# Kernel tuning notes

Hardware: AMD Instinct MI355X
Metric: run time of the kernel (lower is better)

The kernel has to match this reference:

```python
import jax, jax.numpy as jnp
import numpy as np

EMB = 64
N_CONS = 100000
N_VARS = 200000
N_EDGES = 2000000


def _embed(x, shift, scale, W1, b1, W2, b2):
    # PreNormLayer (affine) -> Linear -> ReLU -> Linear -> ReLU
    x = (x - shift) * scale
    x = jax.nn.relu(x @ W1 + b1)
    return jax.nn.relu(x @ W2 + b2)


def _biconv(left, right, ei0, ei1, edge_lin, tgt_idx, n_tgt, tgt_feats,
            Wl, bl, Wr, sf, Wf, bf, sp, Woa, boa, Wob, bob):
    # gather-transform: per-edge joint features [E, EMB]
    joint = (left @ Wl + bl)[ei0] + edge_lin + (right @ Wr)[ei1]
    # feature_module_final: PreNorm(scale-only) -> ReLU -> Linear
    msg = jax.nn.relu(joint * sf) @ Wf + bf
    # scatter-add to target nodes, then post-conv PreNorm(scale-only)
    agg = jax.ops.segment_sum(msg, tgt_idx, num_segments=n_tgt) * sp
    h = jax.nn.relu(jnp.concatenate([agg, tgt_feats], axis=1) @ Woa + boa)
    return h @ Wob + bob


def _forward(constraint_features, edge_features, variable_features,
             c_shift, c_scale, c_W1, c_b1, c_W2, c_b2,
             v_shift, v_scale, v_W1, v_b1, v_W2, v_b2,
             e_shift, e_scale,
             vc_Wl, vc_bl, vc_We, vc_Wr, vc_sf, vc_Wf, vc_bf, vc_sp,
             vc_Woa, vc_boa, vc_Wob, vc_bob,
             cv_Wl, cv_bl, cv_We, cv_Wr, cv_sf, cv_Wf, cv_bf, cv_sp,
             cv_Woa, cv_boa, cv_Wob, cv_bob,
             out_W1, out_b1, out_W2, edge_indices):
    ei0, ei1 = edge_indices[0], edge_indices[1]
    c = _embed(constraint_features, c_shift, c_scale, c_W1, c_b1, c_W2, c_b2)
    v = _embed(variable_features, v_shift, v_scale, v_W1, v_b1, v_W2, v_b2)
    e = (edge_features - e_shift) * e_scale  # edge embedding = PreNorm only, dim 1
    # conv_v_to_c (right_to_left=True): target = constraints via ei0
    c = jax.nn.relu(_biconv(c, v, ei0, ei1, e @ vc_We, ei0, N_CONS, c,
                            vc_Wl, vc_bl, vc_Wr, vc_sf, vc_Wf, vc_bf, vc_sp,
                            vc_Woa, vc_boa, vc_Wob, vc_bob))
    # conv_c_to_v: target = variables via ei1
    v = jax.nn.relu(_biconv(c, v, ei0, ei1, e @ cv_We, ei1, N_VARS, v,
                            cv_Wl, cv_bl, cv_Wr, cv_sf, cv_Wf, cv_bf, cv_sp,
                            cv_Woa, cv_boa, cv_Wob, cv_bob))
    out = jax.nn.relu(v @ out_W1 + out_b1) @ out_W2  # [N_VARS, 1]
    return out.reshape(1, -1)


def setup_inputs():
    key = jax.random.key(0)
    ks = iter(jax.random.split(key, 64))

    def rn(shape, s=0.1):
        return (jax.random.normal(next(ks), shape, jnp.float32) * s).astype(jnp.float32)

    d = {}
    d["constraint_features"] = rn((N_CONS, 5), 1.0)
    d["edge_features"] = rn((N_EDGES, 1), 1.0)
    d["variable_features"] = rn((N_VARS, 19), 1.0)

    def prenorm(n, pre):
        d[pre + "shift"] = rn((n,), 0.05)
        d[pre + "scale"] = jnp.ones((n,), jnp.float32) + rn((n,), 0.05)

    prenorm(5, "c_"); prenorm(19, "v_"); prenorm(1, "e_")
    for pre, nin in (("c_", 5), ("v_", 19)):
        d[pre + "W1"] = rn((nin, EMB)); d[pre + "b1"] = rn((EMB,), 0.02)
        d[pre + "W2"] = rn((EMB, EMB)); d[pre + "b2"] = rn((EMB,), 0.02)
    for pre in ("vc_", "cv_"):
        d[pre + "Wl"] = rn((EMB, EMB)); d[pre + "bl"] = rn((EMB,), 0.02)
        d[pre + "We"] = rn((1, EMB)); d[pre + "Wr"] = rn((EMB, EMB))
        d[pre + "sf"] = jnp.float32(1.0) + rn((), 0.05)
        d[pre + "Wf"] = rn((EMB, EMB)); d[pre + "bf"] = rn((EMB,), 0.02)
        d[pre + "sp"] = jnp.float32(1.0) + rn((), 0.05)
        d[pre + "Woa"] = rn((2 * EMB, EMB)); d[pre + "boa"] = rn((EMB,), 0.02)
        d[pre + "Wob"] = rn((EMB, EMB)); d[pre + "bob"] = rn((EMB,), 0.02)
    d["out_W1"] = rn((EMB, EMB)); d["out_b1"] = rn((EMB,), 0.02)
    d["out_W2"] = rn((EMB, 1))
    d["edge_indices"] = jnp.stack([
        jax.random.randint(next(ks), (N_EDGES,), 0, N_CONS),
        jax.random.randint(next(ks), (N_EDGES,), 0, N_VARS)]).astype(jnp.int32)
    d["n_cons_per_sample"] = jnp.array([N_CONS], jnp.int32)
    d["n_vars_per_sample"] = jnp.array([N_VARS], jnp.int32)
    return d


def reference(constraint_features, edge_features, variable_features,
              c_shift, c_scale, c_W1, c_b1, c_W2, c_b2,
              v_shift, v_scale, v_W1, v_b1, v_W2, v_b2,
              e_shift, e_scale,
              vc_Wl, vc_bl, vc_We, vc_Wr, vc_sf, vc_Wf, vc_bf, vc_sp,
              vc_Woa, vc_boa, vc_Wob, vc_bob,
              cv_Wl, cv_bl, cv_We, cv_Wr, cv_sf, cv_Wf, cv_bf, cv_sp,
              cv_Woa, cv_boa, cv_Wob, cv_bob,
              out_W1, out_b1, out_W2,
              edge_indices, n_cons_per_sample, n_vars_per_sample):
    return _forward(constraint_features, edge_features, variable_features,
                    c_shift, c_scale, c_W1, c_b1, c_W2, c_b2,
                    v_shift, v_scale, v_W1, v_b1, v_W2, v_b2,
                    e_shift, e_scale,
                    vc_Wl, vc_bl, vc_We, vc_Wr, vc_sf, vc_Wf, vc_bf, vc_sp,
                    vc_Woa, vc_boa, vc_Wob, vc_bob,
                    cv_Wl, cv_bl, cv_We, cv_Wr, cv_sf, cv_Wf, cv_bf, cv_sp,
                    cv_Woa, cv_boa, cv_Wob, cv_bob,
                    out_W1, out_b1, out_W2, edge_indices)
```

## Files before the change

kernel.cpp:

```cpp
#include <hip/hip_runtime.h>
#include <hip/hip_bf16.h>

#define DEV __device__ __forceinline__

typedef __attribute__((ext_vector_type(8))) short short8;
typedef __attribute__((ext_vector_type(4))) float f32x4;

DEV unsigned short f2bf(float f) {
    __hip_bfloat16 h = __float2bfloat16(f);
    unsigned short u;
    __builtin_memcpy(&u, &h, 2);
    return u;
}
DEV float bf2f(unsigned short u) { return __uint_as_float((unsigned int)u << 16); }

DEV f32x4 mfma_bf16(short8 a, short8 b, f32x4 c) {
    return __builtin_amdgcn_mfma_f32_16x16x32_bf16(a, b, c, 0, 0, 0);
}

DEV void make_hilo(const float* a8, short8& hi, short8& lo) {
    #pragma unroll
    for (int j = 0; j < 8; ++j) {
        const float v = a8[j];
        const unsigned short h = f2bf(v);
        hi[j] = (short)h;
        lo[j] = (short)f2bf(v - bf2f(h));
    }
}

DEV void mfma3(f32x4 acc[4], short8 ah, short8 al,
               const unsigned short* __restrict__ Bh,
               const unsigned short* __restrict__ Bl,
               int nkt, int tidx, int lane) {
    #pragma unroll
    for (int c = 0; c < 4; ++c) {
        const size_t o = ((size_t)(c * nkt + tidx) * 64 + lane) * 8;
        const short8 bh = *(const short8*)(Bh + o);
        const short8 bl = *(const short8*)(Bl + o);
        acc[c] = mfma_bf16(ah, bh, acc[c]);
        acc[c] = mfma_bf16(al, bh, acc[c]);
        acc[c] = mfma_bf16(ah, bl, acc[c]);
    }
}

DEV int swf(int row, int col) {
    return row * 64 + ((((col >> 3) ^ row) & 7) << 3) + (col & 7);
}

DEV void gemm_lds(f32x4 acc[4], const float* Xl,
                  const unsigned short* Bh, const unsigned short* Bl,
                  int nkt, int t0, int ntk, int l15, int q, int lane) {
    for (int t = 0; t < ntk; ++t) {
        const int ch = (t * 4 + q) ^ (l15 & 7);
        const float* a8 = Xl + l15 * 64 + ch * 8;
        short8 ah, al;
        make_hilo(a8, ah, al);
        mfma3(acc, ah, al, Bh, Bl, nkt, t0 + t, lane);
    }
}

DEV void gemm_glb(f32x4 acc[4], const float* __restrict__ Xg, int rbase, int N,
                  const unsigned short* Bh, const unsigned short* Bl,
                  int nkt, int t0, int ntk, int l15, int q, int lane) {
    const int grow = rbase + l15;
    const bool ok = grow < N;
    for (int t = 0; t < ntk; ++t) {
        float a8[8];
        if (ok) {
            const float4 v0 = *(const float4*)(Xg + (size_t)grow * 64 + t * 32 + q * 8);
            const float4 v1 = *(const float4*)(Xg + (size_t)grow * 64 + t * 32 + q * 8 + 4);
            a8[0] = v0.x; a8[1] = v0.y; a8[2] = v0.z; a8[3] = v0.w;
            a8[4] = v1.x; a8[5] = v1.y; a8[6] = v1.z; a8[7] = v1.w;
        } else {
            #pragma unroll
            for (int j = 0; j < 8; ++j) a8[j] = 0.f;
        }
        short8 ah, al;
        make_hilo(a8, ah, al);
        mfma3(acc, ah, al, Bh, Bl, nkt, t0 + t, lane);
    }
}

#define NMAT 15
struct PrepArgs {
    const float* src[NMAT];
    unsigned short* hi[NMAT];
    unsigned short* lo[NMAT];
    int nkt[NMAT];
    int KR[NMAT];
};

__global__ __launch_bounds__(256)
void prep_kernel(PrepArgs pa)
{
    const int m = blockIdx.y;
    const int nkt = pa.nkt[m];
    const int nthr = nkt * 4 * 64;
    const int p = blockIdx.x * 256 + threadIdx.x;
    if (p >= nthr) return;
    const int f = p >> 6, l = p & 63;
    const int c = f / nkt, t = f % nkt;
    const int kbase = t * 32 + ((l >> 4) << 3);
    const int n = c * 16 + (l & 15);
    const float* W = pa.src[m];
    const int KR = pa.KR[m];
    unsigned short* ph = pa.hi[m] + (size_t)p * 8;
    unsigned short* pl = pa.lo[m] + (size_t)p * 8;
    #pragma unroll
    for (int j = 0; j < 8; ++j) {
        const int k = kbase + j;
        const float v = (k < KR) ? W[k * 64 + n] : 0.f;
        const unsigned short h = f2bf(v);
        ph[j] = h;
        pl[j] = f2bf(v - bf2f(h));
    }
}

struct FusedArgs {
    const int* ei; int E; int nH;
    int* h1; int* h2; unsigned int* rank;
    int tC, tV;
    const float* cf; int NC;
    const float* c_shift; const float* c_scale;
    const float* vf; int NV;
    const float* v_shift; const float* v_scale;
    const unsigned short *cW1h, *cW1l, *cW2h, *cW2l, *cWt1h, *cWt1l;
    const unsigned short *vW1h, *vW1l, *vW2h, *vW2l, *vWt1h, *vWt1l, *vWt2h, *vWt2l;
    const float *c_b1, *c_b2, *v_b1, *v_b2, *vc_bl;
    const float *vc_sf, *cv_sf;
    float* Emc; float* Emv;
    unsigned short* A1; unsigned short* B1; unsigned short* B2;
};

__global__ __launch_bounds__(256)
void fused_he_kernel(FusedArgs a)
{
    __shared__ __align__(16) float Bb[4][1024];

    const int half = blockIdx.x & 1;
    const int idx  = blockIdx.x >> 1;

    if (half == 0) {
        const int stride = a.nH * 256;
        for (int e = idx * 256 + (int)threadIdx.x; e < a.E; e += stride) {
            const int r1 = atomicAdd(a.h1 + a.ei[e], 1);
            const int r2 = atomicAdd(a.h2 + a.ei[a.E + e], 1);
            a.rank[e] = (unsigned int)r1 | ((unsigned int)r2 << 16);
        }
        return;
    }

    int tile = idx;
    const float* x; int N; int IN;
    const float *shift, *scale, *b1, *b2, *bt1;
    const unsigned short *W1h, *W1l, *W2h, *W2l, *Wt1h, *Wt1l;
    const unsigned short *Wt2h = nullptr, *Wt2l = nullptr;
    float* Em; unsigned short* T1; unsigned short* T2 = nullptr;
    float sf1, sf2 = 0.f;
    if (tile < a.tC) {
        x = a.cf; N = a.NC; IN = 5; shift = a.c_shift; scale = a.c_scale;
        W1h = a.cW1h; W1l = a.cW1l; b1 = a.c_b1;
        W2h = a.cW2h; W2l = a.cW2l; b2 = a.c_b2;
        Em = a.Emc; Wt1h = a.cWt1h; Wt1l = a.cWt1l; bt1 = a.vc_bl;
        sf1 = a.vc_sf[0]; T1 = a.A1;
    } else {
        tile -= a.tC;
        x = a.vf; N = a.NV; IN = 19; shift = a.v_shift; scale = a.v_scale;
        W1h = a.vW1h; W1l = a.vW1l; b1 = a.v_b1;
        W2h = a.vW2h; W2l = a.vW2l; b2 = a.v_b2;
        Em = a.Emv; Wt1h = a.vWt1h; Wt1l = a.vWt1l; bt1 = nullptr;
        sf1 = a.vc_sf[0]; T1 = a.B1;
        Wt2h = a.vWt2h; Wt2l = a.vWt2l; sf2 = a.cv_sf[0]; T2 = a.B2;
    }

    const int w = threadIdx.x >> 6, lane = threadIdx.x & 63;
    const int l15 = lane & 15, q = lane >> 4;
    const int rbase = tile * 64 + w * 16;

    {
        f32x4 acc[4] = {{0,0,0,0},{0,0,0,0},{0,0,0,0},{0,0,0,0}};
        const int grow = rbase + l15;
        float a8[8];
        #pragma unroll
        for (int j = 0; j < 8; ++j) {
            const int col = q * 8 + j;
            float v = 0.f;
            if (grow < N && col < IN) v = (x[(size_t)grow * IN + col] - shift[col]) * scale[col];
            a8[j] = v;
        }
        short8 ah, al;
        make_hilo(a8, ah, al);
        mfma3(acc, ah, al, W1h, W1l, 1, 0, lane);
        #pragma unroll
        for (int c = 0; c < 4; ++c) {
            const int col = c * 16 + l15;
            const float bb = b1[col];
            #pragma unroll
            for (int r = 0; r < 4; ++r)
                Bb[w][swf(q * 4 + r, col)] = fmaxf(acc[c][r] + bb, 0.f);
        }
    }
    {
        f32x4 acc[4] = {{0,0,0,0},{0,0,0,0},{0,0,0,0},{0,0,0,0}};
        gemm_lds(acc, Bb[w], W2h, W2l, 2, 0, 2, l15, q, lane);
        #pragma unroll
        for (int c = 0; c < 4; ++c) {
            const int col = c * 16 + l15;
            const float bb = b2[col];
            #pragma unroll
            for (int r = 0; r < 4; ++r) {
                const int row = q * 4 + r;
                const int grow = rbase + row;
                const float v = fmaxf(acc[c][r] + bb, 0.f);
                Bb[w][swf(row, col)] = v;
                if (grow < N) Em[(size_t)grow * 64 + col] = v;
            }
        }
    }
    {
        f32x4 acc[4] = {{0,0,0,0},{0,0,0,0},{0,0,0,0},{0,0,0,0}};
        gemm_lds(acc, Bb[w], Wt1h, Wt1l, 2, 0, 2, l15, q, lane);
        #pragma unroll
        for (int c = 0; c < 4; ++c) {
            const int col = c * 16 + l15;
            const float bb = bt1 ? bt1[col] : 0.f;
            #pragma unroll
            for (int r = 0; r < 4; ++r) {
                const int grow = rbase + q * 4 + r;
                if (grow < N) T1[(size_t)grow * 64 + col] = f2bf(sf1 * (acc[c][r] + bb));
            }
        }
    }
    if (T2 != nullptr) {
        f32x4 acc[4] = {{0,0,0,0},{0,0,0,0},{0,0,0,0},{0,0,0,0}};
        gemm_lds(acc, Bb[w], Wt2h, Wt2l, 2, 0, 2, l15, q, lane);
        #pragma unroll
        for (int c = 0; c < 4; ++c) {
            const int col = c * 16 + l15;
            #pragma unroll
            for (int r = 0; r < 4; ++r) {
                const int grow = rbase + q * 4 + r;
                if (grow < N) T2[(size_t)grow * 64 + col] = f2bf(sf2 * acc[c][r]);
            }
        }
    }
}

template<bool IS_POST2>
__global__ __launch_bounds__(256)
void post_mfma(int N, const float* __restrict__ G, const int* __restrict__ rs,
               const float* __restrict__ Em,
               const unsigned short* __restrict__ Wfh, const unsigned short* __restrict__ Wfl,
               const float* __restrict__ bfv, const float* __restrict__ spp,
               const unsigned short* __restrict__ Woah, const unsigned short* __restrict__ Woal,
               const float* __restrict__ boa,
               const unsigned short* __restrict__ Wobh, const unsigned short* __restrict__ Wobl,
               const float* __restrict__ bob,
               const unsigned short* __restrict__ W4h, const unsigned short* __restrict__ W4l,
               const float* __restrict__ b4,
               const float* __restrict__ sf2p, unsigned short* __restrict__ A2,
               const float* __restrict__ oW2, float* __restrict__ out)
{
    __shared__ __align__(16) float BA[4][1024];
    __shared__ __align__(16) float BB[4][1024];

    const int w = threadIdx.x >> 6, lane = threadIdx.x & 63;
    const int l15 = lane & 15, q = lane >> 4;
    const float sp = spp[0];
    const float sf2 = IS_POST2 ? 0.f : sf2p[0];
    const int rbase = blockIdx.x * 64 + w * 16;

    {
        f32x4 acc[4] = {{0,0,0,0},{0,0,0,0},{0,0,0,0},{0,0,0,0}};
        gemm_glb(acc, G, rbase, N, Wfh, Wfl, 2, 0, 2, l15, q, lane);
        float dgr[4];
        #pragma unroll
        for (int r = 0; r < 4; ++r) {
            const int grow = rbase + q * 4 + r;
            dgr[r] = (grow < N) ? (float)(rs[grow + 1] - rs[grow]) : 0.f;
        }
        #pragma unroll
        for (int c = 0; c < 4; ++c) {
            const int col = c * 16 + l15;
            const float bb = bfv[col];
            #pragma unroll
            for (int r = 0; r < 4; ++r)
                BA[w][swf(q * 4 + r, col)] = (acc[c][r] + dgr[r] * bb) * sp;
        }
    }
    {
        f32x4 acc[4] = {{0,0,0,0},{0,0,0,0},{0,0,0,0},{0,0,0,0}};
        gemm_lds(acc, BA[w], Woah, Woal, 4, 0, 2, l15, q, lane);
        gemm_glb(acc, Em, rbase, N, Woah, Woal, 4, 2, 2, l15, q, lane);
        #pragma unroll
        for (int c = 0; c < 4; ++c) {
            const int col = c * 16 + l15;
            const float bb = boa[col];
            #pragma unroll
            for (int r = 0; r < 4; ++r)
                BB[w][swf(q * 4 + r, col)] = fmaxf(acc[c][r] + bb, 0.f);
        }
    }
    {
        f32x4 acc[4] = {{0,0,0,0},{0,0,0,0},{0,0,0,0},{0,0,0,0}};
        gemm_lds(acc, BB[w], Wobh, Wobl, 2, 0, 2, l15, q, lane);
        #pragma unroll
        for (int c = 0; c < 4; ++c) {
            const int col = c * 16 + l15;
            const float bb = bob[col];
            #pragma unroll
            for (int r = 0; r < 4; ++r)
                BA[w][swf(q * 4 + r, col)] = fmaxf(acc[c][r] + bb, 0.f);
        }
    }
    {
        f32x4 acc[4] = {{0,0,0,0},{0,0,0,0},{0,0,0,0},{0,0,0,0}};
        gemm_lds(acc, BA[w], W4h, W4l, 2, 0, 2, l15, q, lane);
        if (!IS_POST2) {
            #pragma unroll
            for (int c = 0; c < 4; ++c) {
                const int col = c * 16 + l15;
                const float bb = b4[col];
                #pragma unroll
                for (int r = 0; r < 4; ++r) {
                    const int grow = rbase + q * 4 + r;
                    if (grow < N) A2[(size_t)grow * 64 + col] = f2bf(sf2 * (acc[c][r] + bb));
                }
            }
        } else {
            float w2c[4], bb4[4];
            #pragma unroll
            for (int c = 0; c < 4; ++c) {
                const int col = c * 16 + l15;
                w2c[c] = oW2[col];
                bb4[c] = b4[col];
            }
            #pragma unroll
            for (int r = 0; r < 4; ++r) {
                float s = 0.f;
                #pragma unroll
                for (int c = 0; c < 4; ++c)
                    s += fmaxf(acc[c][r] + bb4[c], 0.f) * w2c[c];
                s += __shfl_xor(s, 1);
                s += __shfl_xor(s, 2);
                s += __shfl_xor(s, 4);
                s += __shfl_xor(s, 8);
                const int grow = rbase + q * 4 + r;
                if (l15 == 0 && grow < N) out[grow] = s;
            }
        }
    }
}

__global__ __launch_bounds__(256)
void scanA2_kernel(const int* __restrict__ h1, int n1, int* __restrict__ cs1,
                   const int* __restrict__ h2, int n2, int* __restrict__ cs2)
{
    __shared__ int wsum[4];
    const int which = blockIdx.y;
    const int* h = which ? h2 : h1;
    const int n = which ? n2 : n1;
    int* csum = which ? cs2 : cs1;
    if (blockIdx.x * 4096 >= n) return;

    const int t = threadIdx.x, lane = t & 63, wid = t >> 6;
    const int base = blockIdx.x * 4096 + t * 16;
    int s = 0;
    #pragma unroll
    for (int j = 0; j < 16; ++j) {
        const int idx = base + j;
        if (idx < n) s += h[idx];
    }
    #pragma unroll
    for (int d = 1; d < 64; d <<= 1) s += __shfl_xor(s, d);
    if (lane == 0) wsum[wid] = s;
    __syncthreads();
    if (t == 0) csum[blockIdx.x] = wsum[0] + wsum[1] + wsum[2] + wsum[3];
}

__global__ __launch_bounds__(256)
void scanB2_kernel(int* __restrict__ cs1, int nch1, int* __restrict__ rs1, int n1,
                   int* __restrict__ cs2, int nch2, int* __restrict__ rs2, int n2)
{
    __shared__ int wsum[4];
    const int which = blockIdx.x;
    int* csum = which ? cs2 : cs1;
    const int nchunks = which ? nch2 : nch1;
    int* rs = which ? rs2 : rs1;
    const int n = which ? n2 : n1;

    const int t = threadIdx.x, lane = t & 63, wid = t >> 6;
    const int v = (t < nchunks) ? csum[t] : 0;
    int x = v;
    #pragma unroll
    for (int d = 1; d < 64; d <<= 1) { int y = __shfl_up(x, d); if (lane >= d) x += y; }
    if (lane == 63) wsum[wid] = x;
    __syncthreads();
    int woff = 0;
    for (int i = 0; i < wid; ++i) woff += wsum[i];
    if (t < nchunks) csum[t] = woff + x - v;
    if (t == 0) rs[n] = wsum[0] + wsum[1] + wsum[2] + wsum[3];
}

__global__ __launch_bounds__(256)
void scanC2_kernel(const int* __restrict__ h1, int n1, const int* __restrict__ cs1,
                   int* __restrict__ rs1,
                   const int* __restrict__ h2, int n2, const int* __restrict__ cs2,
                   int* __restrict__ rs2)
{
    __shared__ int wsum[4];
    const int which = blockIdx.y;
    const int* h = which ? h2 : h1;
    const int n = which ? n2 : n1;
    const int* csum = which ? cs2 : cs1;
    int* rs = which ? rs2 : rs1;
    if (blockIdx.x * 4096 >= n) return;

    const int t = threadIdx.x, lane = t & 63, wid = t >> 6;
    const int base = blockIdx.x * 4096 + t * 16;
    int loc[16];
    int s = 0;
    #pragma unroll
    for (int j = 0; j < 16; ++j) {
        loc[j] = s;
        const int idx = base + j;
        if (idx < n) s += h[idx];
    }
    int x = s;
    #pragma unroll
    for (int d = 1; d < 64; d <<= 1) { int y = __shfl_up(x, d); if (lane >= d) x += y; }
    if (lane == 63) wsum[wid] = x;
    __syncthreads();
    int woff = 0;
    for (int i = 0; i < wid; ++i) woff += wsum[i];
    const int toff = csum[blockIdx.x] + woff + x - s;
    #pragma unroll
    for (int j = 0; j < 16; ++j) {
        const int idx = base + j;
        if (idx < n) rs[idx] = toff + loc[j];
    }
}

__global__ __launch_bounds__(256)
void scatter_kernel(const int* __restrict__ ei, int E,
                    const float* __restrict__ ef,
                    const float* __restrict__ eshp, const float* __restrict__ escp,
                    const unsigned int* __restrict__ rank,
                    const int* __restrict__ rs1, const int* __restrict__ rs2,
                    int2* __restrict__ pairs1, int2* __restrict__ pairs2)
{
    const int e = blockIdx.x * 256 + threadIdx.x;
    if (e >= E) return;
    const int i0 = ei[e];
    const int i1 = ei[E + e];
    const unsigned int rk = rank[e];
    const float en = (ef[e] - eshp[0]) * escp[0];
    const int enb = __float_as_int(en);
    const int pos1 = rs1[i0] + (int)(rk & 0xffffu);
    const int pos2 = rs2[i1] + (int)(rk >> 16);
    pairs1[pos1] = make_int2(i1, enb);
    pairs2[pos2] = make_int2(i0, enb);
}

DEV void agg_body(int row, int j, const int* __restrict__ rs,
                  const int2* __restrict__ pairs,
                  const unsigned short* __restrict__ Ttgt,
                  const unsigned short* __restrict__ Tsrc,
                  const float* __restrict__ We, const float* __restrict__ sfp,
                  float* __restrict__ G)
{
    const float base = bf2f(Ttgt[(size_t)row * 64 + j]);
    const float sfWe = sfp[0] * We[j];
    const int s = rs[row];
    const int e = rs[row + 1];
    float acc = 0.f;
    int p = s;
    for (; p + 3 < e; p += 4) {
        const int2 a0 = pairs[p];
        const int2 a1 = pairs[p + 1];
        const int2 a2 = pairs[p + 2];
        const int2 a3 = pairs[p + 3];
        const float b0 = bf2f(Tsrc[(size_t)a0.x * 64 + j]);
        const float b1 = bf2f(Tsrc[(size_t)a1.x * 64 + j]);
        const float b2 = bf2f(Tsrc[(size_t)a2.x * 64 + j]);
        const float b3 = bf2f(Tsrc[(size_t)a3.x * 64 + j]);
        acc += fmaxf(base + b0 + __int_as_float(a0.y) * sfWe, 0.f);
        acc += fmaxf(base + b1 + __int_as_float(a1.y) * sfWe, 0.f);
        acc += fmaxf(base + b2 + __int_as_float(a2.y) * sfWe, 0.f);
        acc += fmaxf(base + b3 + __int_as_float(a3.y) * sfWe, 0.f);
    }
    for (; p < e; ++p) {
        const int2 pr = pairs[p];
        const float bs = bf2f(Tsrc[(size_t)pr.x * 64 + j]);
        acc += fmaxf(base + bs + __int_as_float(pr.y) * sfWe, 0.f);
    }
    G[(size_t)row * 64 + j] = acc;
}

__global__ __launch_bounds__(256)
void agg_kernel(int nrows, const int* __restrict__ rs,
                const int2* __restrict__ pairs,
                const unsigned short* __restrict__ Ttgt,
                const unsigned short* __restrict__ Tsrc,
                const float* __restrict__ We, const float* __restrict__ sfp,
                float* __restrict__ G)
{
    const int row = blockIdx.x * 4 + (int)(threadIdx.x >> 6);
    if (row >= nrows) return;
    agg_body(row, (int)(threadIdx.x & 63), rs, pairs, Ttgt, Tsrc, We, sfp, G);
}

extern "C" void kernel_launch(void* const* d_in, const int* in_sizes, int n_in,
                              void* d_out, int out_size, void* d_ws, size_t ws_size,
                              hipStream_t stream)
{
    const float* cf      = (const float*)d_in[0];
    const float* ef      = (const float*)d_in[1];
    const float* vf      = (const float*)d_in[2];
    const float* c_shift = (const float*)d_in[3];
    const float* c_scale = (const float*)d_in[4];
    const float* v_shift = (const float*)d_in[5];
    const float* v_scale = (const float*)d_in[6];
    const float* e_shift = (const float*)d_in[7];
    const float* e_scale = (const float*)d_in[8];
    const float* c_W1 = (const float*)d_in[9];
    const float* c_b1 = (const float*)d_in[10];
    const float* c_W2 = (const float*)d_in[11];
    const float* c_b2 = (const float*)d_in[12];
    const float* v_W1 = (const float*)d_in[13];
    const float* v_b1 = (const float*)d_in[14];
    const float* v_W2 = (const float*)d_in[15];
    const float* v_b2 = (const float*)d_in[16];
    const float* vc_Wl  = (const float*)d_in[17];
    const float* vc_bl  = (const float*)d_in[18];
    const float* vc_We  = (const float*)d_in[19];
    const float* vc_Wr  = (const float*)d_in[20];
    const float* vc_sf  = (const float*)d_in[21];
    const float* vc_Wf  = (const float*)d_in[22];
    const float* vc_bf  = (const float*)d_in[23];
    const float* vc_sp  = (const float*)d_in[24];
    const float* vc_Woa = (const float*)d_in[25];
    const float* vc_boa = (const float*)d_in[26];
    const float* vc_Wob = (const float*)d_in[27];
    const float* vc_bob = (const float*)d_in[28];
    const float* cv_Wl  = (const float*)d_in[29];
    const float* cv_bl  = (const float*)d_in[30];
    const float* cv_We  = (const float*)d_in[31];
    const float* cv_Wr  = (const float*)d_in[32];
    const float* cv_sf  = (const float*)d_in[33];
    const float* cv_Wf  = (const float*)d_in[34];
    const float* cv_bf  = (const float*)d_in[35];
    const float* cv_sp  = (const float*)d_in[36];
    const float* cv_Woa = (const float*)d_in[37];
    const float* cv_boa = (const float*)d_in[38];
    const float* cv_Wob = (const float*)d_in[39];
    const float* cv_bob = (const float*)d_in[40];
    const float* out_W1 = (const float*)d_in[41];
    const float* out_b1 = (const float*)d_in[42];
    const float* out_W2 = (const float*)d_in[43];
    const int*   eidx   = (const int*)d_in[44];

    const int NC = in_sizes[0] / 5;
    const int NV = in_sizes[2] / 19;
    const int E  = in_sizes[1];

    char* ws = (char*)d_ws;
    size_t off = 0;
    auto alloc = [&](size_t bytes) -> size_t {
        size_t o = off;
        off = (off + bytes + 255) & ~(size_t)255;
        return o;
    };
    size_t o_h1 = alloc((size_t)NC * 4);
    size_t o_h2 = alloc((size_t)NV * 4);
    size_t zero_bytes = off;
    size_t o_rs1  = alloc((size_t)(NC + 1) * 4);
    size_t o_rs2  = alloc((size_t)(NV + 1) * 4);
    size_t o_cs1  = alloc(256 * 4);
    size_t o_cs2  = alloc(256 * 4);
    size_t o_p1   = alloc((size_t)E * 8);
    size_t o_p2   = alloc((size_t)E * 8);
    size_t o_G1   = alloc((size_t)NC * 64 * 4);
    size_t o_G2   = alloc((size_t)NV * 64 * 4);
    size_t o_Emc  = alloc((size_t)NC * 64 * 4);
    size_t o_Emv  = alloc((size_t)NV * 64 * 4);
    size_t o_A1   = alloc((size_t)NC * 64 * 2);
    size_t o_B1   = alloc((size_t)NV * 64 * 2);
    size_t o_B2   = alloc((size_t)NV * 64 * 2);

    static const int nkt_arr[NMAT] = {1,2,2,1,2,2,2,2,4,2,2,2,4,2,2};
    static const int KR_arr[NMAT]  = {5,64,64,19,64,64,64,64,128,64,64,64,128,64,64};
    const float* src_arr[NMAT] = {c_W1, c_W2, vc_Wl, v_W1, v_W2, vc_Wr, cv_Wr,
                                  vc_Wf, vc_Woa, vc_Wob, cv_Wl,
                                  cv_Wf, cv_Woa, cv_Wob, out_W1};
    size_t o_wh[NMAT], o_wl[NMAT];
    for (int m = 0; m < NMAT; ++m) {
        o_wh[m] = alloc((size_t)nkt_arr[m] * 4 * 64 * 8 * 2);
        o_wl[m] = alloc((size_t)nkt_arr[m] * 4 * 64 * 8 * 2);
    }
    (void)ws_size; (void)n_in; (void)out_size;

    int*  h1   = (int*)(ws + o_h1);
    int*  h2   = (int*)(ws + o_h2);
    int*  rs1  = (int*)(ws + o_rs1);
    int*  rs2  = (int*)(ws + o_rs2);
    int*  cs1  = (int*)(ws + o_cs1);
    int*  cs2  = (int*)(ws + o_cs2);
    unsigned int* rank = (unsigned int*)(ws + o_G2);
    int2* p1   = (int2*)(ws + o_p1);
    int2* p2   = (int2*)(ws + o_p2);
    float* G1  = (float*)(ws + o_G1);
    float* G2  = (float*)(ws + o_G2);
    float* Emc = (float*)(ws + o_Emc);
    float* Emv = (float*)(ws + o_Emv);
    unsigned short* A1 = (unsigned short*)(ws + o_A1);
    unsigned short* B1 = (unsigned short*)(ws + o_B1);
    unsigned short* A2 = (unsigned short*)(ws + o_A1);
    unsigned short* B2 = (unsigned short*)(ws + o_B2);

    PrepArgs pa;
    for (int m = 0; m < NMAT; ++m) {
        pa.src[m] = src_arr[m];
        pa.hi[m] = (unsigned short*)(ws + o_wh[m]);
        pa.lo[m] = (unsigned short*)(ws + o_wl[m]);
        pa.nkt[m] = nkt_arr[m];
        pa.KR[m] = KR_arr[m];
    }
    auto WH = [&](int m) { return (const unsigned short*)(ws + o_wh[m]); };
    auto WL = [&](int m) { return (const unsigned short*)(ws + o_wl[m]); };

    hipMemsetAsync(ws, 0, zero_bytes, stream);

    prep_kernel<<<dim3(4, NMAT), 256, 0, stream>>>(pa);

    const int tC = (NC + 63) >> 6, tV = (NV + 63) >> 6;
    const int nE = tC + tV;
    FusedArgs fa;
    fa.ei = eidx; fa.E = E; fa.nH = nE;
    fa.h1 = h1; fa.h2 = h2; fa.rank = rank;
    fa.tC = tC; fa.tV = tV;
    fa.cf = cf; fa.NC = NC; fa.c_shift = c_shift; fa.c_scale = c_scale;
    fa.vf = vf; fa.NV = NV; fa.v_shift = v_shift; fa.v_scale = v_scale;
    fa.cW1h = WH(0); fa.cW1l = WL(0); fa.cW2h = WH(1); fa.cW2l = WL(1);
    fa.cWt1h = WH(2); fa.cWt1l = WL(2);
    fa.vW1h = WH(3); fa.vW1l = WL(3); fa.vW2h = WH(4); fa.vW2l = WL(4);
    fa.vWt1h = WH(5); fa.vWt1l = WL(5); fa.vWt2h = WH(6); fa.vWt2l = WL(6);
    fa.c_b1 = c_b1; fa.c_b2 = c_b2; fa.v_b1 = v_b1; fa.v_b2 = v_b2;
    fa.vc_bl = vc_bl; fa.vc_sf = vc_sf; fa.cv_sf = cv_sf;
    fa.Emc = Emc; fa.Emv = Emv; fa.A1 = A1; fa.B1 = B1; fa.B2 = B2;
    fused_he_kernel<<<2 * nE, 256, 0, stream>>>(fa);

    const int nch1 = (NC + 4095) / 4096, nch2 = (NV + 4095) / 4096;
    const int nchm = nch1 > nch2 ? nch1 : nch2;
    scanA2_kernel<<<dim3(nchm, 2), 256, 0, stream>>>(h1, NC, cs1, h2, NV, cs2);
    scanB2_kernel<<<2, 256, 0, stream>>>(cs1, nch1, rs1, NC, cs2, nch2, rs2, NV);
    scanC2_kernel<<<dim3(nchm, 2), 256, 0, stream>>>(h1, NC, cs1, rs1, h2, NV, cs2, rs2);

    scatter_kernel<<<(E + 255) / 256, 256, 0, stream>>>(
        eidx, E, ef, e_shift, e_scale, rank, rs1, rs2, p1, p2);

    agg_kernel<<<(NC + 3) / 4, 256, 0, stream>>>(
        NC, rs1, p1, A1, B1, vc_We, vc_sf, G1);
    post_mfma<false><<<tC, 256, 0, stream>>>(
        NC, G1, rs1, Emc,
        WH(7), WL(7), vc_bf, vc_sp,
        WH(8), WL(8), vc_boa,
        WH(9), WL(9), vc_bob,
        WH(10), WL(10), cv_bl,
        cv_sf, A2, nullptr, nullptr);

    agg_kernel<<<(NV + 3) / 4, 256, 0, stream>>>(
        NV, rs2, p2, B2, A2, cv_We, cv_sf, G2);
    post_mfma<true><<<tV, 256, 0, stream>>>(
        NV, G2, rs2, Emv,
        WH(11), WL(11), cv_bf, cv_sp,
        WH(12), WL(12), cv_boa,
        WH(13), WL(13), cv_bob,
        WH(14), WL(14), out_b1,
        nullptr, nullptr, out_W2, (float*)d_out);
}
```

Measured before the change: 724.6 us.

## Fuse edge aggregation into post-conv MFMA kernel via LDS staging

Removes the separate agg_kernel and has each wavefront of the post-conv kernel aggregate its 16 target rows directly into LDS, then run the first GEMM from LDS instead of global G. This drops the fp32 G1/G2 intermediate buffers (write and re-read of N*64 floats per conv) and two kernel launches. The inner gather loop is unrolled to 8 edges to expose more memory-level parallelism. In exchange, each wave now processes 16 rows serially, so fewer independent rows are in flight per wave, and degree imbalance within a block can lengthen the tail. The rank buffer gets its own allocation now that G2 is gone.

```diff
diff --git a/kernel.cpp b/kernel.cpp
--- a/kernel.cpp
+++ b/kernel.cpp
@@ -248,18 +248,22 @@
 
 template<bool IS_POST2>
 __global__ __launch_bounds__(256)
-void post_mfma(int N, const float* __restrict__ G, const int* __restrict__ rs,
-               const float* __restrict__ Em,
-               const unsigned short* __restrict__ Wfh, const unsigned short* __restrict__ Wfl,
-               const float* __restrict__ bfv, const float* __restrict__ spp,
-               const unsigned short* __restrict__ Woah, const unsigned short* __restrict__ Woal,
-               const float* __restrict__ boa,
-               const unsigned short* __restrict__ Wobh, const unsigned short* __restrict__ Wobl,
-               const float* __restrict__ bob,
-               const unsigned short* __restrict__ W4h, const unsigned short* __restrict__ W4l,
-               const float* __restrict__ b4,
-               const float* __restrict__ sf2p, unsigned short* __restrict__ A2,
-               const float* __restrict__ oW2, float* __restrict__ out)
+void aggpost_kernel(int N, const int* __restrict__ rs,
+                    const int2* __restrict__ pairs,
+                    const unsigned short* __restrict__ Ttgt,
+                    const unsigned short* __restrict__ Tsrc,
+                    const float* __restrict__ We, const float* __restrict__ sfp,
+                    const float* __restrict__ Em,
+                    const unsigned short* __restrict__ Wfh, const unsigned short* __restrict__ Wfl,
+                    const float* __restrict__ bfv, const float* __restrict__ spp,
+                    const unsigned short* __restrict__ Woah, const unsigned short* __restrict__ Woal,
+                    const float* __restrict__ boa,
+                    const unsigned short* __restrict__ Wobh, const unsigned short* __restrict__ Wobl,
+                    const float* __restrict__ bob,
+                    const unsigned short* __restrict__ W4h, const unsigned short* __restrict__ W4l,
+                    const float* __restrict__ b4,
+                    const float* __restrict__ sf2p, unsigned short* __restrict__ A2,
+                    const float* __restrict__ oW2, float* __restrict__ out)
 {
     __shared__ __align__(16) float BA[4][1024];
     __shared__ __align__(16) float BB[4][1024];
@@ -271,8 +275,40 @@
     const int rbase = blockIdx.x * 64 + w * 16;
 
     {
-        f32x4 acc[4] = {{0,0,0,0},{0,0,0,0},{0,0,0,0},{0,0,0,0}};
-        gemm_glb(acc, G, rbase, N, Wfh, Wfl, 2, 0, 2, l15, q, lane);
+        const float sfWe = sfp[0] * We[lane];
+        for (int r16 = 0; r16 < 16; ++r16) {
+            const int row = rbase + r16;
+            float acc = 0.f;
+            if (row < N) {
+                const float base = bf2f(Ttgt[(size_t)row * 64 + lane]);
+                const int s = rs[row];
+                const int e = rs[row + 1];
+                int p = s;
+                for (; p + 7 < e; p += 8) {
+                    int2 a[8];
+                    float b[8];
+                    #pragma unroll
+                    for (int u = 0; u < 8; ++u) a[u] = pairs[p + u];
+                    #pragma unroll
+                    for (int u = 0; u < 8; ++u)
+                        b[u] = bf2f(Tsrc[(size_t)a[u].x * 64 + lane]);
+                    #pragma unroll
+                    for (int u = 0; u < 8; ++u)
+                        acc += fmaxf(base + b[u] + __int_as_float(a[u].y) * sfWe, 0.f);
+                }
+                for (; p < e; ++p) {
+                    const int2 pr = pairs[p];
+                    const float bs = bf2f(Tsrc[(size_t)pr.x * 64 + lane]);
+                    acc += fmaxf(base + bs + __int_as_float(pr.y) * sfWe, 0.f);
+                }
+            }
+            BA[w][swf(r16, lane)] = acc;
+        }
+    }
+
+    {
+        f32x4 acc[4] = {{0,0,0,0},{0,0,0,0},{0,0,0,0},{0,0,0,0}};
+        gemm_lds(acc, BA[w], Wfh, Wfl, 2, 0, 2, l15, q, lane);
         float dgr[4];
         #pragma unroll
         for (int r = 0; r < 4; ++r) {
@@ -460,54 +496,6 @@
     const int pos2 = rs2[i1] + (int)(rk >> 16);
     pairs1[pos1] = make_int2(i1, enb);
     pairs2[pos2] = make_int2(i0, enb);
-}
-
-DEV void agg_body(int row, int j, const int* __restrict__ rs,
-                  const int2* __restrict__ pairs,
-                  const unsigned short* __restrict__ Ttgt,
-                  const unsigned short* __restrict__ Tsrc,
-                  const float* __restrict__ We, const float* __restrict__ sfp,
-                  float* __restrict__ G)
-{
-    const float base = bf2f(Ttgt[(size_t)row * 64 + j]);
-    const float sfWe = sfp[0] * We[j];
-    const int s = rs[row];
-    const int e = rs[row + 1];
-    float acc = 0.f;
-    int p = s;
-    for (; p + 3 < e; p += 4) {
-        const int2 a0 = pairs[p];
-        const int2 a1 = pairs[p + 1];
-        const int2 a2 = pairs[p + 2];
-        const int2 a3 = pairs[p + 3];
-        const float b0 = bf2f(Tsrc[(size_t)a0.x * 64 + j]);
-        const float b1 = bf2f(Tsrc[(size_t)a1.x * 64 + j]);
-        const float b2 = bf2f(Tsrc[(size_t)a2.x * 64 + j]);
-        const float b3 = bf2f(Tsrc[(size_t)a3.x * 64 + j]);
-        acc += fmaxf(base + b0 + __int_as_float(a0.y) * sfWe, 0.f);
-        acc += fmaxf(base + b1 + __int_as_float(a1.y) * sfWe, 0.f);
-        acc += fmaxf(base + b2 + __int_as_float(a2.y) * sfWe, 0.f);
-        acc += fmaxf(base + b3 + __int_as_float(a3.y) * sfWe, 0.f);
-    }
-    for (; p < e; ++p) {
-        const int2 pr = pairs[p];
-        const float bs = bf2f(Tsrc[(size_t)pr.x * 64 + j]);
-        acc += fmaxf(base + bs + __int_as_float(pr.y) * sfWe, 0.f);
-    }
-    G[(size_t)row * 64 + j] = acc;
-}
-
-__global__ __launch_bounds__(256)
-void agg_kernel(int nrows, const int* __restrict__ rs,
-                const int2* __restrict__ pairs,
-                const unsigned short* __restrict__ Ttgt,
-                const unsigned short* __restrict__ Tsrc,
-                const float* __restrict__ We, const float* __restrict__ sfp,
-                float* __restrict__ G)
-{
-    const int row = blockIdx.x * 4 + (int)(threadIdx.x >> 6);
-    if (row >= nrows) return;
-    agg_body(row, (int)(threadIdx.x & 63), rs, pairs, Ttgt, Tsrc, We, sfp, G);
 }
 
 extern "C" void kernel_launch(void* const* d_in, const int* in_sizes, int n_in,
@@ -578,10 +566,9 @@
     size_t o_rs2  = alloc((size_t)(NV + 1) * 4);
     size_t o_cs1  = alloc(256 * 4);
     size_t o_cs2  = alloc(256 * 4);
+    size_t o_rank = alloc((size_t)E * 4);
     size_t o_p1   = alloc((size_t)E * 8);
     size_t o_p2   = alloc((size_t)E * 8);
-    size_t o_G1   = alloc((size_t)NC * 64 * 4);
-    size_t o_G2   = alloc((size_t)NV * 64 * 4);
     size_t o_Emc  = alloc((size_t)NC * 64 * 4);
     size_t o_Emv  = alloc((size_t)NV * 64 * 4);
     size_t o_A1   = alloc((size_t)NC * 64 * 2);
@@ -606,11 +593,9 @@
     int*  rs2  = (int*)(ws + o_rs2);
     int*  cs1  = (int*)(ws + o_cs1);
     int*  cs2  = (int*)(ws + o_cs2);
-    unsigned int* rank = (unsigned int*)(ws + o_G2);
+    unsigned int* rank = (unsigned int*)(ws + o_rank);
     int2* p1   = (int2*)(ws + o_p1);
     int2* p2   = (int2*)(ws + o_p2);
-    float* G1  = (float*)(ws + o_G1);
-    float* G2  = (float*)(ws + o_G2);
     float* Emc = (float*)(ws + o_Emc);
     float* Emv = (float*)(ws + o_Emv);
     unsigned short* A1 = (unsigned short*)(ws + o_A1);
@@ -659,20 +644,16 @@
     scatter_kernel<<<(E + 255) / 256, 256, 0, stream>>>(
         eidx, E, ef, e_shift, e_scale, rank, rs1, rs2, p1, p2);
 
-    agg_kernel<<<(NC + 3) / 4, 256, 0, stream>>>(
-        NC, rs1, p1, A1, B1, vc_We, vc_sf, G1);
-    post_mfma<false><<<tC, 256, 0, stream>>>(
-        NC, G1, rs1, Emc,
+    aggpost_kernel<false><<<tC, 256, 0, stream>>>(
+        NC, rs1, p1, A1, B1, vc_We, vc_sf, Emc,
         WH(7), WL(7), vc_bf, vc_sp,
         WH(8), WL(8), vc_boa,
         WH(9), WL(9), vc_bob,
         WH(10), WL(10), cv_bl,
         cv_sf, A2, nullptr, nullptr);
 
-    agg_kernel<<<(NV + 3) / 4, 256, 0, stream>>>(
-        NV, rs2, p2, B2, A2, cv_We, cv_sf, G2);
-    post_mfma<true><<<tV, 256, 0, stream>>>(
-        NV, G2, rs2, Emv,
+    aggpost_kernel<true><<<tV, 256, 0, stream>>>(
+        NV, rs2, p2, B2, A2, cv_We, cv_sf, Emv,
         WH(11), WL(11), cv_bf, cv_sp,
         WH(12), WL(12), cv_boa,
         WH(13), WL(13), cv_bob,
```

Result: slower. 835.9 us (+15.4%).
